# Optimization experiments

Measured on AMD Instinct MI355X. Metric: run time of the kernel, lower is better.

## Reference

```python
import jax, jax.numpy as jnp
import numpy as np

N_QUBITS = 12
N_LAYERS = 6
BATCH = 2048
N_OUTPUTS = 2
C64 = jnp.complex64


def setup_inputs() -> dict:
    key = jax.random.key(0)
    k1, k2 = jax.random.split(key)
    x = jax.random.normal(k1, (BATCH, N_QUBITS), dtype=jnp.float32)
    # nn.Parameter: torch.randn(n_layers, n_qubits, 3) * 0.1
    weights = jax.random.normal(k2, (N_LAYERS, N_QUBITS, 3), dtype=jnp.float32) * 0.1
    return {"x": x, "weights": weights}


def _rx(t):
    # t: (...,) angles -> (..., 2, 2) RX matrices
    c = jnp.cos(t * 0.5).astype(C64)
    s = (-1j * jnp.sin(t * 0.5)).astype(C64)
    return jnp.stack([jnp.stack([c, s], -1), jnp.stack([s, c], -1)], -2)


def _ry(t):
    c = jnp.cos(t * 0.5).astype(C64)
    s = jnp.sin(t * 0.5).astype(C64)
    return jnp.stack([jnp.stack([c, -s], -1), jnp.stack([s, c], -1)], -2)


def _rz(t):
    e = jnp.exp(-0.5j * t).astype(C64)
    z = jnp.zeros_like(e)
    return jnp.stack([jnp.stack([e, z], -1), jnp.stack([z, jnp.conj(e)], -1)], -2)


def _rot(w):
    # PennyLane Rot(phi, theta, omega) = RZ(omega) @ RY(theta) @ RZ(phi); w: (n_qubits, 3)
    return _rz(w[:, 2]) @ _ry(w[:, 1]) @ _rz(w[:, 0])


def _apply_1q(state, gate, q):
    # state: (B, 2**n) complex; gate: (2,2) or (B,2,2); qubit q (wire 0 = MSB)
    B = state.shape[0]
    s = state.reshape(B, 2 ** q, 2, -1)
    if gate.ndim == 3:
        s = jnp.einsum('bij,bljr->blir', gate, s)
    else:
        s = jnp.einsum('ij,bljr->blir', gate, s)
    return s.reshape(B, -1)


def _apply_cnot(state, c, t, n):
    # control c, target t; flip target axis where control bit == 1
    B = state.shape[0]
    s = state.reshape((B,) + (2,) * n)
    ac, at = 1 + c, 1 + t
    s0 = jnp.take(s, 0, axis=ac)
    s1 = jnp.take(s, 1, axis=ac)
    at2 = at - 1 if at > ac else at
    s1 = jnp.flip(s1, axis=at2)
    s = jnp.stack([s0, s1], axis=ac)
    return s.reshape(B, -1)


def _layer(state, w, n):
    # strongly-entangling layer: Rot on every wire, then full CNOT entanglement
    rot = _rot(w)  # (n, 2, 2)
    for q in range(n):
        state = _apply_1q(state, rot[q], q)
    for i in range(n):
        for j in range(i + 1, n):
            state = _apply_cnot(state, i, j, n)
    return state


def _forward(x, weights):
    n = N_QUBITS
    B = x.shape[0]
    state = jnp.zeros((B, 2 ** n), C64).at[:, 0].set(1.0)
    # angle encoding: RX(x_q) on wire q (PennyLane AngleEmbedding default axis X)
    for q in range(n):
        state = _apply_1q(state, _rx(x[:, q]), q)
    layer_ckpt = jax.checkpoint(lambda s, w: _layer(s, w, n))
    for l in range(N_LAYERS):
        state = layer_ckpt(state, weights[l])
    # expval(PauliZ) on wires 0..n_outputs-1
    probs = state.real ** 2 + state.imag ** 2  # (B, 2**n)
    outs = []
    for k in range(N_OUTPUTS):
        p = probs.reshape(B, 2 ** k, 2, -1)
        outs.append(p[:, :, 0, :].sum((1, 2)) - p[:, :, 1, :].sum((1, 2)))
    return jnp.stack(outs, -1)  # (B, n_outputs)


def reference(x, weights):
    return _forward(x, weights)
```

## Files before the change

### kernel.cpp

```cpp
#include <hip/hip_runtime.h>
#include <math.h>

#define NQ 12
#define DIM 4096
#define NL 6
#define TPB 256

typedef float f2 __attribute__((ext_vector_type(2)));


__device__ __forceinline__ f2 pk_mul(f2 a, f2 b) {
  f2 d; asm("v_pk_mul_f32 %0, %1, %2" : "=v"(d) : "v"(a), "v"(b)); return d;
}
__device__ __forceinline__ f2 pk_fma(f2 a, f2 b, f2 c) {
  f2 d; asm("v_pk_fma_f32 %0, %1, %2, %3" : "=v"(d) : "v"(a), "v"(b), "v"(c)); return d;
}
__device__ __forceinline__ f2 cmulp(f2 a, f2 c) {
  f2 r1, d;
  asm("v_pk_mul_f32 %0, %1, %2 op_sel:[0,0] op_sel_hi:[0,1]"
      : "=v"(r1) : "v"(a), "v"(c));
  asm("v_pk_fma_f32 %0, %1, %2, %3 op_sel:[1,1,0] op_sel_hi:[1,0,1] neg_lo:[1,0,0]"
      : "=v"(d) : "v"(a), "v"(c), "v"(r1));
  return d;
}
__device__ __forceinline__ f2 cj(f2 a) { return (f2){a.x, -a.y}; }

template<int BIT>
__device__ __forceinline__ void apply_ry16(f2 v[16], f2 cc, f2 ss) {
  #pragma unroll
  for (int j = 0; j < 16; ++j) {
    if (j & (1 << BIT)) continue;
    const int k = j | (1 << BIT);
    f2 a = v[j], b = v[k];
    f2 t1 = pk_mul(a, cc);
    f2 t2 = pk_mul(a, ss);
    f2 na; asm("v_pk_fma_f32 %0, %1, %2, %3 neg_lo:[1,0,0] neg_hi:[1,0,0]"
               : "=v"(na) : "v"(b), "v"(ss), "v"(t1));
    f2 nb = pk_fma(b, cc, t2);
    v[j] = na; v[k] = nb;
  }
}

__global__ __launch_bounds__(TPB, 4)
void qsim12_kernel(const float* __restrict__ x, const float* __restrict__ w,
                   float* __restrict__ out) {
  __shared__ __align__(16) float st[2*DIM];

  const int t = threadIdx.x;
  const int b = blockIdx.x;
  char* stb = (char*)st;
  const int lane = t & 63;

  int baseA[8], baseB[8];
  #pragma unroll
  for (int m = 0; m < 8; ++m) {
    baseA[m] = (t << 7) + (((2*m) ^ (t & 14)) << 3);
    baseB[m] = ((t >> 4) << 11) + ((((t & 15) ^ (2*m))) << 3);
  }
  const int baseC = ((t >> 4) << 7) + ((((t & 15) ^ ((t >> 4) & 15))) << 3);
  const int G = t ^ (t >> 1);
  int baseS[2];
  #pragma unroll
  for (int par = 0; par < 2; ++par) {
    const int k8 = par << 3;
    baseS[par] = ((((G >> 4) & 15) ^ k8) << 7)
               + ((((G & 15) ^ ((G >> 4) & 14) ^ k8)) << 3);
  }
  float sg[8];
  #pragma unroll
  for (int k = 0; k < 8; ++k) sg[k] = ((t >> k) & 1) ? 0.5f : -0.5f;

  f2 v[16];

  {
    float cw[NQ], sw[NQ];
    #pragma unroll
    for (int q = 0; q < NQ; ++q) {
      float xv = 0.5f * x[b*NQ + q];
      sincosf(xv, &sw[q], &cw[q]);
    }
    float rhi = 1.f;
    #pragma unroll
    for (int k = 0; k < 8; ++k)
      rhi *= ((t >> k) & 1) ? sw[7-k] : cw[7-k];
    const int popt = __popc(t);
    #pragma unroll
    for (int j = 0; j < 16; ++j) {
      float r = rhi;
      #pragma unroll
      for (int m = 0; m < 4; ++m)
        r *= ((j >> m) & 1) ? sw[11-m] : cw[11-m];
      const int pj = (popt + __popc(j)) & 3;
      if      (pj == 0) v[j] = (f2){ r, 0.f};
      else if (pj == 1) v[j] = (f2){0.f, -r};
      else if (pj == 2) v[j] = (f2){-r, 0.f};
      else              v[j] = (f2){0.f,  r};
    }
  }

  #define BC(S)  (f2){ __shfl(cv_s, (S)), __shfl(sv_s, (S)) }
  #define RYG(BIT, WQ)                                                \
    { float c = __shfl(cv_s, (WQ)), s = __shfl(sv_s, (WQ));           \
      apply_ry16<BIT>(v, (f2){c, c}, (f2){s, s}); }

  #pragma unroll 1
  for (int l = 0; l < NL; ++l) {
    const float* wl = w + l*NQ*3;

    float cv_s, sv_s;
    {
      int slot = (lane < 20) ? lane : 0;
      float ang;
      if (slot < 12)      ang = 0.5f * wl[slot*3 + 1];
      else if (slot < 16) ang = 0.5f * wl[(23 - slot)*3 + 0];
      else                ang = 0.5f * wl[(19 - slot)*3 + 2];
      sincosf(ang, &sv_s, &cv_s);
    }

    if (l > 0) {
      #pragma unroll
      for (int m = 0; m < 8; ++m) {
        float4 q4 = *(const float4*)(stb + baseA[m]);
        v[2*m]   = (f2){q4.x, q4.y};
        v[2*m+1] = (f2){q4.z, q4.w};
      }
    }
    {
      f2 p0 = BC(12), p1 = BC(13), p2 = BC(14), p3 = BC(15);
      float fa = 0.f;
      #pragma unroll
      for (int k = 0; k < 8; ++k) fa += sg[k] * wl[(7-k)*3 + 0];
      float was, wac; sincosf(fa, &was, &wac);
      f2 wA = (f2){wac, was};
      f2 z01[4] = { cmulp(cj(p0), cj(p1)), cmulp(p0, cj(p1)),
                    cmulp(cj(p0), p1),     cmulp(p0, p1) };
      f2 w2m = cmulp(cj(p2), wA), w2p = cmulp(p2, wA);
      f2 z23[4] = { cmulp(w2m, cj(p3)), cmulp(w2p, cj(p3)),
                    cmulp(w2m, p3),     cmulp(w2p, p3) };
      #pragma unroll
      for (int j = 0; j < 16; ++j)
        v[j] = cmulp(cmulp(v[j], z01[j & 3]), z23[j >> 2]);
    }
    RYG(0,11) RYG(1,10) RYG(2,9) RYG(3,8)
    #pragma unroll
    for (int m = 0; m < 8; ++m)
      *(float4*)(stb + baseA[m]) =
          make_float4(v[2*m].x, v[2*m].y, v[2*m+1].x, v[2*m+1].y);
    __syncthreads();

    #pragma unroll
    for (int m = 0; m < 8; ++m) {
      v[2*m]   = *(const f2*)(stb + baseB[m] + (2*m)*128);
      v[2*m+1] = *(const f2*)(stb + baseB[m] + (2*m+1)*128);
    }
    RYG(0,7) RYG(1,6) RYG(2,5) RYG(3,4)
    #pragma unroll
    for (int m = 0; m < 8; ++m) {
      *(f2*)(stb + baseB[m] + (2*m)*128)         = v[2*m];
      *(f2*)(stb + (baseB[m] ^ 8) + (2*m+1)*128) = v[2*m+1];
    }
    __syncthreads();

    #pragma unroll
    for (int j = 0; j < 16; ++j)
      v[j] = *(const f2*)(stb + baseC + j*2048);
    RYG(0,3) RYG(1,2) RYG(2,1) RYG(3,0)
    if (l < NL-1) {
      {
        f2 q0 = BC(16), q1 = BC(17), q2 = BC(18), q3 = BC(19);
        float fc = 0.f;
        #pragma unroll
        for (int k = 0; k < 8; ++k) fc += sg[k] * wl[(11-k)*3 + 2];
        float wcs, wcc; sincosf(fc, &wcs, &wcc);
        f2 wC = (f2){wcc, wcs};
        f2 z01[4] = { cmulp(cj(q0), cj(q1)), cmulp(q0, cj(q1)),
                      cmulp(cj(q0), q1),     cmulp(q0, q1) };
        f2 w2m = cmulp(cj(q2), wC), w2p = cmulp(q2, wC);
        f2 z23[4] = { cmulp(w2m, cj(q3)), cmulp(w2p, cj(q3)),
                      cmulp(w2m, q3),     cmulp(w2p, q3) };
        #pragma unroll
        for (int j = 0; j < 16; ++j)
          v[j] = cmulp(cmulp(v[j], z01[j & 3]), z23[j >> 2]);
      }
      #pragma unroll
      for (int j = 0; j < 16; ++j) {
        const int g4 = (j ^ (j >> 1)) & 15;
        *(f2*)(stb + baseS[j & 1] + (g4 << 11)) = v[j];
      }
      __syncthreads();
    }
  }

  float a0 = 0.f, a1 = 0.f;
  #pragma unroll
  for (int j = 0; j < 16; ++j) {
    float pr = v[j].x*v[j].x + v[j].y*v[j].y;
    a0 += ((j >> 3) & 1) ? -pr : pr;
    a1 += (((j >> 2) ^ (j >> 3)) & 1) ? -pr : pr;
  }
  #pragma unroll
  for (int off = 32; off >= 1; off >>= 1) {
    a0 += __shfl_down(a0, off);
    a1 += __shfl_down(a1, off);
  }
  __syncthreads();
  if ((t & 63) == 0) { st[(t >> 6)*2] = a0; st[(t >> 6)*2 + 1] = a1; }
  __syncthreads();
  if (t == 0) {
    out[b*2 + 0] = st[0] + st[2] + st[4] + st[6];
    out[b*2 + 1] = st[1] + st[3] + st[5] + st[7];
  }
}

extern "C" void kernel_launch(void* const* d_in, const int* in_sizes, int n_in,
                              void* d_out, int out_size, void* d_ws, size_t ws_size,
                              hipStream_t stream) {
  const float* x = (const float*)d_in[0];
  const float* w = (const float*)d_in[1];
  float* out = (float*)d_out;
  int B = in_sizes[0] / NQ;
  qsim12_kernel<<<B, TPB, 0, stream>>>(x, w, out);
}
```

Before: 144.1 us.

## Process two batch elements per block to amortize gate setup and syncs

Each block now simulates two batch samples at once, holding two 16-amplitude register sets and a doubled shared-memory buffer. Gate coefficients (sincos, shuffles, phase products) and barriers are shared across both samples, and the grid is halved. This doubles register pressure and LDS per block (launch bounds lowered to 2), which reduces occupancy and assumes an even batch size.

```diff
diff --git a/kernel.cpp b/kernel.cpp
--- a/kernel.cpp
+++ b/kernel.cpp
@@ -41,13 +41,13 @@
   }
 }
 
-__global__ __launch_bounds__(TPB, 4)
+__global__ __launch_bounds__(TPB, 2)
 void qsim12_kernel(const float* __restrict__ x, const float* __restrict__ w,
                    float* __restrict__ out) {
-  __shared__ __align__(16) float st[2*DIM];
+  __shared__ __align__(16) float st[4*DIM];
 
   const int t = threadIdx.x;
-  const int b = blockIdx.x;
+  const int b0 = blockIdx.x * 2;
   char* stb = (char*)st;
   const int lane = t & 63;
 
@@ -70,38 +70,51 @@
   #pragma unroll
   for (int k = 0; k < 8; ++k) sg[k] = ((t >> k) & 1) ? 0.5f : -0.5f;
 
-  f2 v[16];
+  f2 v0[16], v1[16];
 
   {
-    float cw[NQ], sw[NQ];
-    #pragma unroll
-    for (int q = 0; q < NQ; ++q) {
-      float xv = 0.5f * x[b*NQ + q];
-      sincosf(xv, &sw[q], &cw[q]);
-    }
-    float rhi = 1.f;
-    #pragma unroll
-    for (int k = 0; k < 8; ++k)
-      rhi *= ((t >> k) & 1) ? sw[7-k] : cw[7-k];
+    float cxv, sxv;
+    {
+      int slot = (lane < 24) ? lane : 0;
+      int e = (slot >= 12) ? 1 : 0;
+      int q = slot - 12*e;
+      float ang = 0.5f * x[(b0 + e)*NQ + q];
+      sincosf(ang, &sxv, &cxv);
+    }
     const int popt = __popc(t);
-    #pragma unroll
-    for (int j = 0; j < 16; ++j) {
-      float r = rhi;
-      #pragma unroll
-      for (int m = 0; m < 4; ++m)
-        r *= ((j >> m) & 1) ? sw[11-m] : cw[11-m];
-      const int pj = (popt + __popc(j)) & 3;
-      if      (pj == 0) v[j] = (f2){ r, 0.f};
-      else if (pj == 1) v[j] = (f2){0.f, -r};
-      else if (pj == 2) v[j] = (f2){-r, 0.f};
-      else              v[j] = (f2){0.f,  r};
-    }
+    #define INIT_ELEM(VV, OFS)                                           \
+    { float cw[NQ], sw[NQ];                                              \
+      _Pragma("unroll")                                                  \
+      for (int q = 0; q < NQ; ++q) {                                     \
+        cw[q] = __shfl(cxv, (OFS) + q);                                  \
+        sw[q] = __shfl(sxv, (OFS) + q);                                  \
+      }                                                                  \
+      float rhi = 1.f;                                                   \
+      _Pragma("unroll")                                                  \
+      for (int k = 0; k < 8; ++k)                                        \
+        rhi *= ((t >> k) & 1) ? sw[7-k] : cw[7-k];                       \
+      _Pragma("unroll")                                                  \
+      for (int j = 0; j < 16; ++j) {                                     \
+        float r = rhi;                                                   \
+        _Pragma("unroll")                                                \
+        for (int m = 0; m < 4; ++m)                                      \
+          r *= ((j >> m) & 1) ? sw[11-m] : cw[11-m];                     \
+        const int pj = (popt + __popc(j)) & 3;                           \
+        if      (pj == 0) VV[j] = (f2){ r, 0.f};                         \
+        else if (pj == 1) VV[j] = (f2){0.f, -r};                         \
+        else if (pj == 2) VV[j] = (f2){-r, 0.f};                         \
+        else              VV[j] = (f2){0.f,  r};                         \
+      } }
+    INIT_ELEM(v0, 0)
+    INIT_ELEM(v1, 12)
   }
 
   #define BC(S)  (f2){ __shfl(cv_s, (S)), __shfl(sv_s, (S)) }
   #define RYG(BIT, WQ)                                                \
     { float c = __shfl(cv_s, (WQ)), s = __shfl(sv_s, (WQ));           \
-      apply_ry16<BIT>(v, (f2){c, c}, (f2){s, s}); }
+      f2 cc = (f2){c, c}, ss = (f2){s, s};                            \
+      apply_ry16<BIT>(v0, cc, ss);                                    \
+      apply_ry16<BIT>(v1, cc, ss); }
 
   #pragma unroll 1
   for (int l = 0; l < NL; ++l) {
@@ -121,8 +134,11 @@
       #pragma unroll
       for (int m = 0; m < 8; ++m) {
         float4 q4 = *(const float4*)(stb + baseA[m]);
-        v[2*m]   = (f2){q4.x, q4.y};
-        v[2*m+1] = (f2){q4.z, q4.w};
+        v0[2*m]   = (f2){q4.x, q4.y};
+        v0[2*m+1] = (f2){q4.z, q4.w};
+        float4 q5 = *(const float4*)(stb + baseA[m] + 32768);
+        v1[2*m]   = (f2){q5.x, q5.y};
+        v1[2*m+1] = (f2){q5.z, q5.w};
       }
     }
     {
@@ -138,32 +154,43 @@
       f2 z23[4] = { cmulp(w2m, cj(p3)), cmulp(w2p, cj(p3)),
                     cmulp(w2m, p3),     cmulp(w2p, p3) };
       #pragma unroll
-      for (int j = 0; j < 16; ++j)
-        v[j] = cmulp(cmulp(v[j], z01[j & 3]), z23[j >> 2]);
+      for (int j = 0; j < 16; ++j) {
+        v0[j] = cmulp(cmulp(v0[j], z01[j & 3]), z23[j >> 2]);
+        v1[j] = cmulp(cmulp(v1[j], z01[j & 3]), z23[j >> 2]);
+      }
     }
     RYG(0,11) RYG(1,10) RYG(2,9) RYG(3,8)
     #pragma unroll
-    for (int m = 0; m < 8; ++m)
+    for (int m = 0; m < 8; ++m) {
       *(float4*)(stb + baseA[m]) =
-          make_float4(v[2*m].x, v[2*m].y, v[2*m+1].x, v[2*m+1].y);
+          make_float4(v0[2*m].x, v0[2*m].y, v0[2*m+1].x, v0[2*m+1].y);
+      *(float4*)(stb + baseA[m] + 32768) =
+          make_float4(v1[2*m].x, v1[2*m].y, v1[2*m+1].x, v1[2*m+1].y);
+    }
     __syncthreads();
 
     #pragma unroll
     for (int m = 0; m < 8; ++m) {
-      v[2*m]   = *(const f2*)(stb + baseB[m] + (2*m)*128);
-      v[2*m+1] = *(const f2*)(stb + baseB[m] + (2*m+1)*128);
+      v0[2*m]   = *(const f2*)(stb + baseB[m] + (2*m)*128);
+      v0[2*m+1] = *(const f2*)(stb + baseB[m] + (2*m+1)*128);
+      v1[2*m]   = *(const f2*)(stb + baseB[m] + (2*m)*128 + 32768);
+      v1[2*m+1] = *(const f2*)(stb + baseB[m] + (2*m+1)*128 + 32768);
     }
     RYG(0,7) RYG(1,6) RYG(2,5) RYG(3,4)
     #pragma unroll
     for (int m = 0; m < 8; ++m) {
-      *(f2*)(stb + baseB[m] + (2*m)*128)         = v[2*m];
-      *(f2*)(stb + (baseB[m] ^ 8) + (2*m+1)*128) = v[2*m+1];
+      *(f2*)(stb + baseB[m] + (2*m)*128)                 = v0[2*m];
+      *(f2*)(stb + (baseB[m] ^ 8) + (2*m+1)*128)         = v0[2*m+1];
+      *(f2*)(stb + baseB[m] + (2*m)*128 + 32768)         = v1[2*m];
+      *(f2*)(stb + (baseB[m] ^ 8) + (2*m+1)*128 + 32768) = v1[2*m+1];
     }
     __syncthreads();
 
     #pragma unroll
-    for (int j = 0; j < 16; ++j)
-      v[j] = *(const f2*)(stb + baseC + j*2048);
+    for (int j = 0; j < 16; ++j) {
+      v0[j] = *(const f2*)(stb + baseC + j*2048);
+      v1[j] = *(const f2*)(stb + baseC + j*2048 + 32768);
+    }
     RYG(0,3) RYG(1,2) RYG(2,1) RYG(3,0)
     if (l < NL-1) {
       {
@@ -179,36 +206,49 @@
         f2 z23[4] = { cmulp(w2m, cj(q3)), cmulp(w2p, cj(q3)),
                       cmulp(w2m, q3),     cmulp(w2p, q3) };
         #pragma unroll
-        for (int j = 0; j < 16; ++j)
-          v[j] = cmulp(cmulp(v[j], z01[j & 3]), z23[j >> 2]);
+        for (int j = 0; j < 16; ++j) {
+          v0[j] = cmulp(cmulp(v0[j], z01[j & 3]), z23[j >> 2]);
+          v1[j] = cmulp(cmulp(v1[j], z01[j & 3]), z23[j >> 2]);
+        }
       }
       #pragma unroll
       for (int j = 0; j < 16; ++j) {
         const int g4 = (j ^ (j >> 1)) & 15;
-        *(f2*)(stb + baseS[j & 1] + (g4 << 11)) = v[j];
+        *(f2*)(stb + baseS[j & 1] + (g4 << 11))         = v0[j];
+        *(f2*)(stb + baseS[j & 1] + (g4 << 11) + 32768) = v1[j];
       }
       __syncthreads();
     }
   }
 
-  float a0 = 0.f, a1 = 0.f;
+  float a0 = 0.f, a1 = 0.f, a2 = 0.f, a3 = 0.f;
   #pragma unroll
   for (int j = 0; j < 16; ++j) {
-    float pr = v[j].x*v[j].x + v[j].y*v[j].y;
-    a0 += ((j >> 3) & 1) ? -pr : pr;
-    a1 += (((j >> 2) ^ (j >> 3)) & 1) ? -pr : pr;
+    const float s0 = ((j >> 3) & 1) ? -1.f : 1.f;
+    const float s1 = (((j >> 2) ^ (j >> 3)) & 1) ? -1.f : 1.f;
+    float p0 = v0[j].x*v0[j].x + v0[j].y*v0[j].y;
+    float p1 = v1[j].x*v1[j].x + v1[j].y*v1[j].y;
+    a0 += s0 * p0;  a1 += s1 * p0;
+    a2 += s0 * p1;  a3 += s1 * p1;
   }
   #pragma unroll
   for (int off = 32; off >= 1; off >>= 1) {
     a0 += __shfl_down(a0, off);
     a1 += __shfl_down(a1, off);
+    a2 += __shfl_down(a2, off);
+    a3 += __shfl_down(a3, off);
   }
   __syncthreads();
-  if ((t & 63) == 0) { st[(t >> 6)*2] = a0; st[(t >> 6)*2 + 1] = a1; }
+  if ((t & 63) == 0) {
+    st[(t >> 6)*2 + 0] = a0;  st[(t >> 6)*2 + 1] = a1;
+    st[8 + (t >> 6)*2 + 0] = a2;  st[8 + (t >> 6)*2 + 1] = a3;
+  }
   __syncthreads();
   if (t == 0) {
-    out[b*2 + 0] = st[0] + st[2] + st[4] + st[6];
-    out[b*2 + 1] = st[1] + st[3] + st[5] + st[7];
+    out[b0*2 + 0] = st[0] + st[2] + st[4] + st[6];
+    out[b0*2 + 1] = st[1] + st[3] + st[5] + st[7];
+    out[b0*2 + 2] = st[8]  + st[10] + st[12] + st[14];
+    out[b0*2 + 3] = st[9]  + st[11] + st[13] + st[15];
   }
 }
 
@@ -219,5 +259,5 @@
   const float* w = (const float*)d_in[1];
   float* out = (float*)d_out;
   int B = in_sizes[0] / NQ;
-  qsim12_kernel<<<B, TPB, 0, stream>>>(x, w, out);
-}
+  qsim12_kernel<<<B/2, TPB, 0, stream>>>(x, w, out);
+}
```

After: 150.2 us. 4.2% more time.
